# Optimization experiments

Hardware: AMD Instinct MI355X
Metric: run time of the kernel (lower is better)

## Reference

```python
import jax, jax.numpy as jnp
import numpy as np

H = 32        # num_attention_heads
KVH = 8       # num_key_value_heads
D = 2048      # hidden_size
HD = D // H   # head_dim = 64
GROUPS = H // KVH


def setup_inputs() -> dict:
    key = jax.random.key(0)
    k1, k2, k3, k4 = jax.random.split(key, 4)
    B, T = 2, 2048
    x = jax.random.normal(k1, (B, T, D), dtype=jnp.float32)
    wq = jax.random.normal(k2, (D, H * HD), dtype=jnp.float32) * (D ** -0.5)
    wkv = jax.random.normal(k3, (D, 2 * KVH * HD), dtype=jnp.float32) * (D ** -0.5)
    wo = jax.random.normal(k4, (H * HD, D), dtype=jnp.float32) * (D ** -0.5)
    return {"x": x, "wq": wq, "wkv": wkv, "wo": wo}


def reference(x, wq, wkv, wo):
    B, T, _ = x.shape
    scale = HD ** -0.5
    # projections
    q = (x @ wq).reshape(B, T, H, HD).transpose(0, 2, 1, 3)        # [B,H,T,hd]
    kv = x @ wkv                                                    # [B,T,2*KVH*hd]
    k, v = jnp.split(kv, 2, axis=-1)
    k = k.reshape(B, T, KVH, HD).transpose(0, 2, 1, 3)              # [B,KVH,T,hd]
    v = v.reshape(B, T, KVH, HD).transpose(0, 2, 1, 3)
    # repeat_interleave KV heads to match Q heads
    k = jnp.repeat(k, GROUPS, axis=1)                               # [B,H,T,hd]
    v = jnp.repeat(v, GROUPS, axis=1)
    scores = jnp.einsum('bhqd,bhkd->bhqk', q, k) * scale            # [B,H,T,T]
    causal = jnp.triu(jnp.ones((T, T), dtype=bool), k=1)
    scores = jnp.where(causal, -jnp.inf, scores)
    attn = jax.nn.softmax(scores, axis=-1)
    out = jnp.einsum('bhqk,bhkd->bhqd', attn, v)                    # [B,H,T,hd]
    out = out.transpose(0, 2, 1, 3).reshape(B, T, H * HD)
    return out @ wo
```

## Files before the change

### kernel.cpp

```cpp
#include <hip/hip_runtime.h>

using bf16   = __bf16;
using bf16x8 = __attribute__((ext_vector_type(8))) __bf16;
using f32x4  = __attribute__((ext_vector_type(4))) float;

#define T_SEQ 2048
#define NQKV 3072

__device__ __forceinline__ void async_cp16(const bf16* g, bf16* l) {
  __builtin_amdgcn_global_load_lds((__attribute__((address_space(1))) void*)(void*)g,
                                   (__attribute__((address_space(3))) void*)l, 16, 0, 0);
}

__global__ __launch_bounds__(256) void cvt_kernel(const float* __restrict__ in,
                                                  bf16* __restrict__ out) {
  long i = ((long)blockIdx.x * 256 + threadIdx.x) * 8;
  float4 a = *(const float4*)(in + i);
  float4 c = *(const float4*)(in + i + 4);
  bf16x8 v;
  v[0] = (bf16)a.x; v[1] = (bf16)a.y; v[2] = (bf16)a.z; v[3] = (bf16)a.w;
  v[4] = (bf16)c.x; v[5] = (bf16)c.y; v[6] = (bf16)c.z; v[7] = (bf16)c.w;
  *(bf16x8*)(out + i) = v;
}

__global__ __launch_bounds__(256) void transpose_cvt(const float* __restrict__ in,
                                                     bf16* __restrict__ out,
                                                     int R, int C) {
  __shared__ float tile[32][33];
  const int tc = blockIdx.x * 32;
  const int tr = blockIdx.y * 32;
  const int t = threadIdx.x;
  const int lr = t >> 5;
  const int lc = t & 31;
#pragma unroll
  for (int i = 0; i < 4; ++i)
    tile[lr + i * 8][lc] = in[(size_t)(tr + lr + i * 8) * C + tc + lc];
  __syncthreads();
#pragma unroll
  for (int i = 0; i < 4; ++i)
    out[(size_t)(tc + lr + i * 8) * R + tr + lc] = (bf16)tile[lc][lr + i * 8];
}

__global__ __launch_bounds__(256) void transpose_v(const bf16* __restrict__ in,
                                                   bf16* __restrict__ out) {
  __shared__ bf16 tile[32][33];
  const int c0 = blockIdx.x * 32;
  const int r0 = blockIdx.y * 32;
  const int t = threadIdx.x;
  const int lr = t >> 5;
  const int lc = t & 31;
#pragma unroll
  for (int i = 0; i < 4; ++i)
    tile[lr + i * 8][lc] = in[(size_t)(r0 + lr + i * 8) * NQKV + 2560 + c0 + lc];
  __syncthreads();
#pragma unroll
  for (int i = 0; i < 4; ++i) {
    int c = c0 + lr + i * 8;
    int r = r0 + lc;
    out[(size_t)((r >> 11) * 512 + c) * 2048 + (r & 2047)] = tile[lc][lr + i * 8];
  }
}

template <bool OUT_BF16>
__global__ __launch_bounds__(256, 3)
void gemm_kernel(const bf16* __restrict__ A, const bf16* __restrict__ Bt,
                 void* __restrict__ Cout, int Kdim, int Ndim) {
  __shared__ __attribute__((aligned(16))) bf16 As[128 * 64];
  __shared__ __attribute__((aligned(16))) bf16 Bs[128 * 64];
  const int tid  = threadIdx.x;
  const int lane = tid & 63;
  const int wave = tid >> 6;
  const int l16  = lane & 15;
  const int q4   = lane >> 4;
  const long m0 = (long)blockIdx.y * 128;
  const long n0 = (long)blockIdx.x * 128;
  const int wm = (wave >> 1) * 64;
  const int wn = (wave & 1) * 64;

  f32x4 acc[4][4] = {};

  for (int k0 = 0; k0 < Kdim; k0 += 64) {
    __syncthreads();
#pragma unroll
    for (int rr = 0; rr < 4; ++rr) {
      int ci  = rr * 256 + tid;
      int row = ci >> 3;
      int chp = ci & 7;
      int ch  = chp ^ (row & 7);
      async_cp16(A + (m0 + row) * (long)Kdim + k0 + ch * 8, &As[ci * 8]);
      async_cp16(Bt + (n0 + row) * (long)Kdim + k0 + ch * 8, &Bs[ci * 8]);
    }
    __syncthreads();
#pragma unroll
    for (int ks = 0; ks < 2; ++ks) {
      bf16x8 af[4], bfr[4];
#pragma unroll
      for (int mt = 0; mt < 4; ++mt) {
        int row = wm + mt * 16 + l16;
        int chp = (ks * 4 + q4) ^ (row & 7);
        af[mt] = *(const bf16x8*)&As[row * 64 + chp * 8];
      }
#pragma unroll
      for (int nt = 0; nt < 4; ++nt) {
        int row = wn + nt * 16 + l16;
        int chp = (ks * 4 + q4) ^ (row & 7);
        bfr[nt] = *(const bf16x8*)&Bs[row * 64 + chp * 8];
      }
#pragma unroll
      for (int mt = 0; mt < 4; ++mt)
#pragma unroll
        for (int nt = 0; nt < 4; ++nt)
          acc[mt][nt] = __builtin_amdgcn_mfma_f32_16x16x32_bf16(af[mt], bfr[nt],
                                                                acc[mt][nt], 0, 0, 0);
    }
  }
#pragma unroll
  for (int mt = 0; mt < 4; ++mt)
#pragma unroll
    for (int nt = 0; nt < 4; ++nt)
#pragma unroll
      for (int r = 0; r < 4; ++r) {
        long row = m0 + wm + mt * 16 + q4 * 4 + r;
        long col = n0 + wn + nt * 16 + l16;
        float v = acc[mt][nt][r];
        if constexpr (OUT_BF16)
          ((bf16*)Cout)[row * Ndim + col] = (bf16)v;
        else
          ((float*)Cout)[row * Ndim + col] = v;
      }
}

__global__ __launch_bounds__(256, 3)
void attn_kernel(const bf16* __restrict__ qkv, const bf16* __restrict__ vT,
                 bf16* __restrict__ outb) {
  __shared__ __attribute__((aligned(16))) bf16 Ks[64 * 64];
  __shared__ __attribute__((aligned(16))) bf16 Vs[64 * 64];
  __shared__ __attribute__((aligned(16))) bf16 Ps[4][32 * 72];

  const int tid  = threadIdx.x;
  const int lane = tid & 63;
  const int wave = tid >> 6;
  const int l16  = lane & 15;
  const int q4   = lane >> 4;

  const int bid = blockIdx.x;
  const int qt  = 15 - (bid >> 6);
  const int bh  = bid & 63;
  const int b   = bh >> 5;
  const int h   = bh & 31;
  const int kvh = h >> 2;
  const long rowbase = (long)b * T_SEQ;

  const int qrow0 = qt * 128;
  const int wq0   = qrow0 + wave * 32;
  const float cexp = 0.125f * 1.4426950408889634f;

  bf16x8 aq[2][2];
#pragma unroll
  for (int mt = 0; mt < 2; ++mt)
#pragma unroll
    for (int ks = 0; ks < 2; ++ks) {
      bf16x8 v = *(const bf16x8*)(qkv +
          (rowbase + wq0 + mt * 16 + l16) * (long)NQKV + h * 64 + ks * 32 + q4 * 8);
#pragma unroll
      for (int i = 0; i < 8; ++i) v[i] = (bf16)((float)v[i] * cexp);
      aq[mt][ks] = v;
    }

  bf16x8 ones_f;
#pragma unroll
  for (int i = 0; i < 8; ++i) ones_f[i] = (l16 == 0) ? (bf16)1.0f : (bf16)0.0f;

  f32x4 o[2][4] = {};
  f32x4 o_l[2] = {};

  const bf16* kbase = qkv + rowbase * (long)NQKV + 2048 + kvh * 64;
  const bf16* vbase = vT + ((long)b * 512 + kvh * 64) * 2048;

  for (int j0 = 0; j0 < qrow0 + 128; j0 += 64) {
    __syncthreads();
    {
#pragma unroll
      for (int h2 = 0; h2 < 2; ++h2) {
        int ci  = h2 * 256 + tid;
        int row = ci >> 3;
        int ch  = (ci & 7) ^ (row & 7);
        *(bf16x8*)&Ks[ci * 8] =
            *(const bf16x8*)(kbase + (long)(j0 + row) * NQKV + ch * 8);
        *(bf16x8*)&Vs[ci * 8] =
            *(const bf16x8*)(vbase + (long)row * 2048 + j0 + ch * 8);
      }
    }
    __syncthreads();
    if (j0 > wq0 + 31) continue;

    f32x4 s[2][4] = {};
#pragma unroll
    for (int ks = 0; ks < 2; ++ks) {
      bf16x8 bk[4];
#pragma unroll
      for (int nt = 0; nt < 4; ++nt) {
        int row  = nt * 16 + l16;
        int slot = (ks * 4 + q4) ^ (row & 7);
        bk[nt] = *(const bf16x8*)&Ks[row * 64 + slot * 8];
      }
#pragma unroll
      for (int mt = 0; mt < 2; ++mt)
#pragma unroll
        for (int nt = 0; nt < 4; ++nt)
          s[mt][nt] = __builtin_amdgcn_mfma_f32_16x16x32_bf16(aq[mt][ks], bk[nt],
                                                              s[mt][nt], 0, 0, 0);
    }

    if (j0 + 63 > wq0) {
#pragma unroll
      for (int mt = 0; mt < 2; ++mt)
#pragma unroll
        for (int nt = 0; nt < 4; ++nt)
#pragma unroll
          for (int r = 0; r < 4; ++r) {
            int rg = wq0 + mt * 16 + q4 * 4 + r;
            int cg = j0 + nt * 16 + l16;
            if (cg > rg) s[mt][nt][r] = -__builtin_inff();
          }
    }

#pragma unroll
    for (int mt = 0; mt < 2; ++mt)
#pragma unroll
      for (int nt = 0; nt < 4; ++nt)
#pragma unroll
        for (int r = 0; r < 4; ++r) {
          float pv = exp2f(s[mt][nt][r]);
          Ps[wave][(mt * 16 + q4 * 4 + r) * 72 + nt * 16 + l16] = (bf16)pv;
        }

#pragma unroll
    for (int ks = 0; ks < 2; ++ks) {
      bf16x8 ap[2], bv[4];
#pragma unroll
      for (int mt = 0; mt < 2; ++mt)
        ap[mt] = *(const bf16x8*)&Ps[wave][(mt * 16 + l16) * 72 + ks * 32 + q4 * 8];
#pragma unroll
      for (int dt = 0; dt < 4; ++dt) {
        int row  = dt * 16 + l16;
        int slot = (ks * 4 + q4) ^ (row & 7);
        bv[dt] = *(const bf16x8*)&Vs[row * 64 + slot * 8];
      }
#pragma unroll
      for (int mt = 0; mt < 2; ++mt) {
#pragma unroll
        for (int dt = 0; dt < 4; ++dt)
          o[mt][dt] = __builtin_amdgcn_mfma_f32_16x16x32_bf16(ap[mt], bv[dt],
                                                              o[mt][dt], 0, 0, 0);
        o_l[mt] = __builtin_amdgcn_mfma_f32_16x16x32_bf16(ap[mt], ones_f,
                                                          o_l[mt], 0, 0, 0);
      }
    }
  }

#pragma unroll
  for (int mt = 0; mt < 2; ++mt) {
    float inv[4];
#pragma unroll
    for (int r = 0; r < 4; ++r) {
      float lsum = __shfl(o_l[mt][r], lane & 48);
      inv[r] = 1.0f / lsum;
    }
#pragma unroll
    for (int dt = 0; dt < 4; ++dt)
#pragma unroll
      for (int r = 0; r < 4; ++r) {
        long row = rowbase + wq0 + mt * 16 + q4 * 4 + r;
        int col = h * 64 + dt * 16 + l16;
        outb[row * 2048 + col] = (bf16)(o[mt][dt][r] * inv[r]);
      }
  }
}

extern "C" void kernel_launch(void* const* d_in, const int* in_sizes, int n_in,
                              void* d_out, int out_size, void* d_ws, size_t ws_size,
                              hipStream_t stream) {
  const float* x   = (const float*)d_in[0];
  const float* wq  = (const float*)d_in[1];
  const float* wkv = (const float*)d_in[2];
  const float* wo  = (const float*)d_in[3];
  float* out = (float*)d_out;
  char* ws = (char*)d_ws;

  bf16* xbf  = (bf16*)(ws + 0);
  bf16* w1   = (bf16*)(ws + 16777216);
  bf16* qkv  = (bf16*)(ws + 29360128);
  bf16* attn = xbf;
  bf16* vT   = w1;

  const size_t need_parallel = 54525952u + 8388608u;
  bf16* woT;
  bool woT_early;
  if (ws_size >= need_parallel) {
    woT = (bf16*)(ws + 54525952);
    woT_early = true;
  } else {
    woT = qkv;
    woT_early = false;
  }

  cvt_kernel<<<4096, 256, 0, stream>>>(x, xbf);
  transpose_cvt<<<dim3(64, 64), 256, 0, stream>>>(wq, w1, 2048, 2048);
  transpose_cvt<<<dim3(32, 64), 256, 0, stream>>>(wkv, w1 + 2048L * 2048, 2048, 1024);
  if (woT_early)
    transpose_cvt<<<dim3(64, 64), 256, 0, stream>>>(wo, woT, 2048, 2048);

  gemm_kernel<true><<<dim3(24, 32), 256, 0, stream>>>(xbf, w1, (void*)qkv, 2048, 3072);

  transpose_v<<<dim3(16, 128), 256, 0, stream>>>(qkv, vT);

  attn_kernel<<<1024, 256, 0, stream>>>(qkv, vT, attn);

  if (!woT_early)
    transpose_cvt<<<dim3(64, 64), 256, 0, stream>>>(wo, woT, 2048, 2048);

  gemm_kernel<false><<<dim3(16, 32), 256, 0, stream>>>(attn, woT, (void*)out, 2048, 2048);
}
```

Before: 274.3 us.

## Fuse V transpose into QKV GEMM epilogue and merge prep kernels

The QKV GEMM's V-column blocks now transpose their tile through LDS and write V^T directly, so the separate transpose_v pass and the V columns in the qkv buffer are gone (row stride shrinks to 2560). The input conversion and the weight transposes are merged into one prep_kernel launch. V^T is staged in the output buffer to save workspace. The aim is fewer launches and less global memory traffic. The cost is a larger LDS footprint in the GEMM and more branching in the epilogue.

```diff
diff --git a/kernel.cpp b/kernel.cpp
--- a/kernel.cpp
+++ b/kernel.cpp
@@ -5,68 +5,73 @@
 using f32x4  = __attribute__((ext_vector_type(4))) float;
 
 #define T_SEQ 2048
-#define NQKV 3072
+#define QKS 2560
 
 __device__ __forceinline__ void async_cp16(const bf16* g, bf16* l) {
   __builtin_amdgcn_global_load_lds((__attribute__((address_space(1))) void*)(void*)g,
                                    (__attribute__((address_space(3))) void*)l, 16, 0, 0);
 }
 
-__global__ __launch_bounds__(256) void cvt_kernel(const float* __restrict__ in,
-                                                  bf16* __restrict__ out) {
-  long i = ((long)blockIdx.x * 256 + threadIdx.x) * 8;
-  float4 a = *(const float4*)(in + i);
-  float4 c = *(const float4*)(in + i + 4);
-  bf16x8 v;
-  v[0] = (bf16)a.x; v[1] = (bf16)a.y; v[2] = (bf16)a.z; v[3] = (bf16)a.w;
-  v[4] = (bf16)c.x; v[5] = (bf16)c.y; v[6] = (bf16)c.z; v[7] = (bf16)c.w;
-  *(bf16x8*)(out + i) = v;
+__device__ __forceinline__ void transpose_body(const float* __restrict__ in,
+                                               bf16* __restrict__ out,
+                                               int bx, int by, int R, int C) {
+  __shared__ float tile[32][33];
+  const int tc = bx * 32;
+  const int tr = by * 32;
+  const int t = threadIdx.x;
+  const int lr = t >> 5;
+  const int lc = t & 31;
+#pragma unroll
+  for (int i = 0; i < 4; ++i)
+    tile[lr + i * 8][lc] = in[(size_t)(tr + lr + i * 8) * C + tc + lc];
+  __syncthreads();
+#pragma unroll
+  for (int i = 0; i < 4; ++i)
+    out[(size_t)(tc + lr + i * 8) * R + tr + lc] = (bf16)tile[lc][lr + i * 8];
+}
+
+__global__ __launch_bounds__(256) void prep_kernel(const float* __restrict__ x,
+                                                   const float* __restrict__ wq,
+                                                   const float* __restrict__ wkv,
+                                                   const float* __restrict__ wo,
+                                                   bf16* __restrict__ xbf,
+                                                   bf16* __restrict__ w1,
+                                                   bf16* __restrict__ woT) {
+  const int i = blockIdx.x;
+  if (i < 4096) {
+    long e = ((long)i * 256 + threadIdx.x) * 8;
+    float4 a = *(const float4*)(x + e);
+    float4 c = *(const float4*)(x + e + 4);
+    bf16x8 v;
+    v[0] = (bf16)a.x; v[1] = (bf16)a.y; v[2] = (bf16)a.z; v[3] = (bf16)a.w;
+    v[4] = (bf16)c.x; v[5] = (bf16)c.y; v[6] = (bf16)c.z; v[7] = (bf16)c.w;
+    *(bf16x8*)(xbf + e) = v;
+  } else if (i < 8192) {
+    int idx = i - 4096;
+    transpose_body(wq, w1, idx & 63, idx >> 6, 2048, 2048);
+  } else if (i < 10240) {
+    int idx = i - 8192;
+    transpose_body(wkv, w1 + 2048L * 2048, idx & 31, idx >> 5, 2048, 1024);
+  } else {
+    int idx = i - 10240;
+    transpose_body(wo, woT, idx & 63, idx >> 6, 2048, 2048);
+  }
 }
 
 __global__ __launch_bounds__(256) void transpose_cvt(const float* __restrict__ in,
                                                      bf16* __restrict__ out,
                                                      int R, int C) {
-  __shared__ float tile[32][33];
-  const int tc = blockIdx.x * 32;
-  const int tr = blockIdx.y * 32;
-  const int t = threadIdx.x;
-  const int lr = t >> 5;
-  const int lc = t & 31;
-#pragma unroll
-  for (int i = 0; i < 4; ++i)
-    tile[lr + i * 8][lc] = in[(size_t)(tr + lr + i * 8) * C + tc + lc];
-  __syncthreads();
-#pragma unroll
-  for (int i = 0; i < 4; ++i)
-    out[(size_t)(tc + lr + i * 8) * R + tr + lc] = (bf16)tile[lc][lr + i * 8];
-}
-
-__global__ __launch_bounds__(256) void transpose_v(const bf16* __restrict__ in,
-                                                   bf16* __restrict__ out) {
-  __shared__ bf16 tile[32][33];
-  const int c0 = blockIdx.x * 32;
-  const int r0 = blockIdx.y * 32;
-  const int t = threadIdx.x;
-  const int lr = t >> 5;
-  const int lc = t & 31;
-#pragma unroll
-  for (int i = 0; i < 4; ++i)
-    tile[lr + i * 8][lc] = in[(size_t)(r0 + lr + i * 8) * NQKV + 2560 + c0 + lc];
-  __syncthreads();
-#pragma unroll
-  for (int i = 0; i < 4; ++i) {
-    int c = c0 + lr + i * 8;
-    int r = r0 + lc;
-    out[(size_t)((r >> 11) * 512 + c) * 2048 + (r & 2047)] = tile[lc][lr + i * 8];
-  }
-}
-
-template <bool OUT_BF16>
+  transpose_body(in, out, blockIdx.x, blockIdx.y, R, C);
+}
+
+template <bool OUT_BF16, bool V_TRANS>
 __global__ __launch_bounds__(256, 3)
 void gemm_kernel(const bf16* __restrict__ A, const bf16* __restrict__ Bt,
-                 void* __restrict__ Cout, int Kdim, int Ndim) {
-  __shared__ __attribute__((aligned(16))) bf16 As[128 * 64];
-  __shared__ __attribute__((aligned(16))) bf16 Bs[128 * 64];
+                 void* __restrict__ Cout, int Kdim, int Ndim,
+                 bf16* __restrict__ vTout) {
+  __shared__ __attribute__((aligned(16))) bf16 smem[17408];
+  bf16* As = smem;
+  bf16* Bs = smem + 8192;
   const int tid  = threadIdx.x;
   const int lane = tid & 63;
   const int wave = tid >> 6;
@@ -114,6 +119,32 @@
                                                                 acc[mt][nt], 0, 0, 0);
     }
   }
+
+  if constexpr (V_TRANS) {
+    if (blockIdx.x >= 20) {
+      __syncthreads();
+#pragma unroll
+      for (int mt = 0; mt < 4; ++mt)
+#pragma unroll
+        for (int nt = 0; nt < 4; ++nt)
+#pragma unroll
+          for (int r = 0; r < 4; ++r) {
+            int rl = wm + mt * 16 + q4 * 4 + r;
+            int cl = wn + nt * 16 + l16;
+            smem[cl * 132 + rl] = (bf16)acc[mt][nt][r];
+          }
+      __syncthreads();
+      int cl = tid >> 1, half = tid & 1;
+      long vrow = (m0 >> 11) * 512 + (n0 - 2560) + cl;
+      bf16* dst = vTout + vrow * 2048 + (m0 & 2047) + half * 64;
+      const bf16* src = &smem[cl * 132 + half * 64];
+#pragma unroll
+      for (int j = 0; j < 8; ++j)
+        *(bf16x8*)(dst + j * 8) = *(const bf16x8*)(src + j * 8);
+      return;
+    }
+  }
+
 #pragma unroll
   for (int mt = 0; mt < 4; ++mt)
 #pragma unroll
@@ -161,7 +192,7 @@
 #pragma unroll
     for (int ks = 0; ks < 2; ++ks) {
       bf16x8 v = *(const bf16x8*)(qkv +
-          (rowbase + wq0 + mt * 16 + l16) * (long)NQKV + h * 64 + ks * 32 + q4 * 8);
+          (rowbase + wq0 + mt * 16 + l16) * (long)QKS + h * 64 + ks * 32 + q4 * 8);
 #pragma unroll
       for (int i = 0; i < 8; ++i) v[i] = (bf16)((float)v[i] * cexp);
       aq[mt][ks] = v;
@@ -174,7 +205,7 @@
   f32x4 o[2][4] = {};
   f32x4 o_l[2] = {};
 
-  const bf16* kbase = qkv + rowbase * (long)NQKV + 2048 + kvh * 64;
+  const bf16* kbase = qkv + rowbase * (long)QKS + 2048 + kvh * 64;
   const bf16* vbase = vT + ((long)b * 512 + kvh * 64) * 2048;
 
   for (int j0 = 0; j0 < qrow0 + 128; j0 += 64) {
@@ -186,7 +217,7 @@
         int row = ci >> 3;
         int ch  = (ci & 7) ^ (row & 7);
         *(bf16x8*)&Ks[ci * 8] =
-            *(const bf16x8*)(kbase + (long)(j0 + row) * NQKV + ch * 8);
+            *(const bf16x8*)(kbase + (long)(j0 + row) * QKS + ch * 8);
         *(bf16x8*)&Vs[ci * 8] =
             *(const bf16x8*)(vbase + (long)row * 2048 + j0 + ch * 8);
       }
@@ -292,33 +323,30 @@
   bf16* w1   = (bf16*)(ws + 16777216);
   bf16* qkv  = (bf16*)(ws + 29360128);
   bf16* attn = xbf;
-  bf16* vT   = w1;
-
-  const size_t need_parallel = 54525952u + 8388608u;
+  bf16* vT   = (bf16*)d_out;
+
+  const size_t need_parallel = 50331648u + 8388608u;
   bf16* woT;
   bool woT_early;
   if (ws_size >= need_parallel) {
-    woT = (bf16*)(ws + 54525952);
+    woT = (bf16*)(ws + 50331648);
     woT_early = true;
   } else {
     woT = qkv;
     woT_early = false;
   }
 
-  cvt_kernel<<<4096, 256, 0, stream>>>(x, xbf);
-  transpose_cvt<<<dim3(64, 64), 256, 0, stream>>>(wq, w1, 2048, 2048);
-  transpose_cvt<<<dim3(32, 64), 256, 0, stream>>>(wkv, w1 + 2048L * 2048, 2048, 1024);
-  if (woT_early)
-    transpose_cvt<<<dim3(64, 64), 256, 0, stream>>>(wo, woT, 2048, 2048);
-
-  gemm_kernel<true><<<dim3(24, 32), 256, 0, stream>>>(xbf, w1, (void*)qkv, 2048, 3072);
-
-  transpose_v<<<dim3(16, 128), 256, 0, stream>>>(qkv, vT);
+  prep_kernel<<<woT_early ? 14336 : 10240, 256, 0, stream>>>(x, wq, wkv, wo,
+                                                             xbf, w1, woT);
+
+  gemm_kernel<true, true><<<dim3(24, 32), 256, 0, stream>>>(xbf, w1, (void*)qkv,
+                                                            2048, 2560, vT);
 
   attn_kernel<<<1024, 256, 0, stream>>>(qkv, vT, attn);
 
   if (!woT_early)
     transpose_cvt<<<dim3(64, 64), 256, 0, stream>>>(wo, woT, 2048, 2048);
 
-  gemm_kernel<false><<<dim3(16, 32), 256, 0, stream>>>(attn, woT, (void*)out, 2048, 2048);
-}
+  gemm_kernel<false, false><<<dim3(16, 32), 256, 0, stream>>>(attn, woT, (void*)out,
+                                                              2048, 2048, nullptr);
+}
```

New measurement: 276.8 us. About the same (+0.9%).
